# Kernel tuning notes

Measured on AMD Instinct MI355X. Metric: run time of the kernel, lower is better.

Reference implementation:

```python
import jax, jax.numpy as jnp
import numpy as np

B, C, H, W = 32, 256, 56, 56
NUM_ITER = 5

# Row-major upper-triangular (incl. diagonal) flat indices, matching
# torch.ones(C, C).triu().view(-1).nonzero() in the original triuvec.
_r, _c = np.triu_indices(C)
TRIU_IDX = jnp.asarray(_r * C + _c)


def setup_inputs() -> dict:
    key = jax.random.key(0)
    x = jax.random.normal(key, (B, C, H, W), dtype=jnp.float32)
    return {"x": x}


def _cov_pool(x):
    # x: (b, c, h, w) -> sigma = x_n @ ((1/n) I - (1/n^2) J) @ x_n^T : (b, c, c)
    b, c, h, w = x.shape
    n = h * w
    xn = x.reshape(b, c, n)
    s = xn.sum(axis=2)  # (b, c) = x_n @ ones
    gram = jnp.einsum('bcn,bdn->bcd', xn, xn)  # (b, c, c)
    return gram / n - jnp.einsum('bc,bd->bcd', s, s) / (n * n)


def _newton_schulz_sqrt(x, num_iter):
    # x: (b, m, m) SPD; returns approx matrix square root, scaled by sqrt(trace).
    b, m, _ = x.shape
    eye = jnp.eye(m, dtype=x.dtype)
    x_trace = jnp.trace(x, axis1=1, axis2=2)[:, None, None]  # (b, 1, 1)
    a = x / x_trace
    i3 = 3.0 * eye  # broadcasts over batch
    # iteration 0
    b2 = 0.5 * (i3 - a)
    yi = a @ b2
    zi = b2

    def body(carry, _):
        yi, zi = carry
        b2 = 0.5 * (i3 - zi @ yi)
        return (yi @ b2, b2 @ zi), None

    (yi, zi), _ = jax.lax.scan(body, (yi, zi), None, length=num_iter - 1)
    return yi * jnp.sqrt(x_trace)


def _triuvec(x):
    # (b, c, c) -> (b, c*(c+1)//2), row-major upper triangle incl. diagonal
    b, c, _ = x.shape
    return x.reshape(b, c * c)[:, TRIU_IDX]


def reference(x) -> jnp.ndarray:
    cov = _cov_pool(x)
    y = _newton_schulz_sqrt(cov, NUM_ITER)
    return _triuvec(y)
```

## Files before the change

### kernel.cpp

```cpp
#include <hip/hip_runtime.h>
#include <hip/hip_bf16.h>
#include <math.h>

#define BATCH 32
#define C 256
#define HW 3136
#define OUTROW 32896
#define KSPLIT 7
#define KCHUNK 448
#define KC32 98


typedef __bf16 b8v __attribute__((ext_vector_type(8)));
typedef float  f4v __attribute__((ext_vector_type(4)));

__device__ __forceinline__ unsigned short f2bf(float f) {
    union { float f; unsigned u; } v; v.f = f;
    unsigned r = v.u + 0x7FFFu + ((v.u >> 16) & 1u);
    return (unsigned short)(r >> 16);
}
__device__ __forceinline__ float bf2f(unsigned short h) {
    union { unsigned u; float f; } v; v.u = ((unsigned)h) << 16; return v.f;
}
__device__ __forceinline__ void split2(float x, unsigned short& h, unsigned short& l) {
    h = f2bf(x);
    l = f2bf(x - bf2f(h));
}

__device__ __forceinline__ float wave_sum(float v) {
    for (int o = 32; o; o >>= 1) v += __shfl_down(v, o, 64);
    return v;
}

__global__ void k_prep(const float* __restrict__ x, unsigned short* __restrict__ xh,
                       unsigned short* __restrict__ xl, float* __restrict__ sbuf,
                       float* __restrict__ qbuf) {
    const int row = blockIdx.x;
    const int b = row >> 8, c = row & 255;
    const float4* xr = (const float4*)(x + (size_t)row * HW);
    float s = 0.f, q = 0.f;
    for (int idx = threadIdx.x; idx < HW / 4; idx += 256) {
        const int k = idx * 4;
        const int kc = k >> 5, ko = k & 31;
        float4 v = xr[idx];
        ushort4 h, l;
        split2(v.x, h.x, l.x); split2(v.y, h.y, l.y);
        split2(v.z, h.z, l.z); split2(v.w, h.w, l.w);
        const size_t dst = ((size_t)(b * KC32 + kc) * 256 + c) * 32 + ko;
        *(ushort4*)&xh[dst] = h;
        *(ushort4*)&xl[dst] = l;
        s += v.x + v.y + v.z + v.w;
        q += v.x * v.x + v.y * v.y + v.z * v.z + v.w * v.w;
    }
    s = wave_sum(s); q = wave_sum(q);
    __shared__ float ss[4], qq[4];
    if ((threadIdx.x & 63) == 0) { ss[threadIdx.x >> 6] = s; qq[threadIdx.x >> 6] = q; }
    __syncthreads();
    if (threadIdx.x == 0) {
        sbuf[row] = ss[0] + ss[1] + ss[2] + ss[3];
        qbuf[row] = qq[0] + qq[1] + qq[2] + qq[3];
    }
}

__global__ void k_tr(const float* __restrict__ sbuf, const float* __restrict__ qbuf,
                     float* __restrict__ trbuf, float* __restrict__ strbuf) {
    const int b = blockIdx.x, t = threadIdx.x;
    const float invn = 1.f / (float)HW, invn2 = invn * invn;
    float sv = sbuf[b * C + t];
    float v = qbuf[b * C + t] * invn - sv * sv * invn2;
    v = wave_sum(v);
    __shared__ float red[4];
    if ((t & 63) == 0) red[t >> 6] = v;
    __syncthreads();
    if (t == 0) {
        float tr = red[0] + red[1] + red[2] + red[3];
        trbuf[b] = tr;
        strbuf[b] = sqrtf(tr);
    }
}

__global__ __launch_bounds__(64) void k_gram_split(
    const unsigned short* __restrict__ Xh, const unsigned short* __restrict__ Xl,
    float* __restrict__ part) {
    const int bid = blockIdx.x;
    const int x8 = bid & 7;
    const int t8 = bid >> 3;
    const int pairIdx = t8 % 10;
    const int g = (t8 / 10) * 8 + x8;
    const int b = g & 31;
    const int z = g >> 5;

    int p = pairIdx, tm = 0, rem = 4;
    while (p >= rem) { p -= rem; ++tm; --rem; }
    const int tn = tm + p;

    const int lane = threadIdx.x & 63;
    const int q = lane >> 4, r = lane & 15;
    const int kc0 = z * (KCHUNK / 32);
    const size_t matb = (size_t)b * KC32 * 8192;

    int oA[4], oB[4];
#pragma unroll
    for (int i = 0; i < 4; ++i) {
        oA[i] = (tm * 64 + i * 16 + r) * 32 + q * 8;
        oB[i] = (tn * 64 + i * 16 + r) * 32 + q * 8;
    }

    f4v acc[4][4] = {};
    b8v fAh[2][4], fAl[2][4], fBh[2][4], fBl[2][4];
#define LDG(buf, kc)                                                     \
    do {                                                                 \
        const size_t sb = matb + (size_t)(kc0 + (kc)) * 8192;            \
        for (int i = 0; i < 4; ++i) {                                    \
            fAh[buf][i] = *(const b8v*)(Xh + sb + oA[i]);                \
            fAl[buf][i] = *(const b8v*)(Xl + sb + oA[i]);                \
            fBh[buf][i] = *(const b8v*)(Xh + sb + oB[i]);                \
            fBl[buf][i] = *(const b8v*)(Xl + sb + oB[i]);                \
        }                                                                \
    } while (0)

    LDG(0, 0);
#pragma unroll
    for (int kc = 0; kc < KCHUNK / 32; ++kc) {
        const int cb = kc & 1, nb = cb ^ 1;
        if (kc < KCHUNK / 32 - 1) LDG(nb, kc + 1);
#pragma unroll
        for (int i = 0; i < 4; ++i)
#pragma unroll
            for (int j = 0; j < 4; ++j) {
                acc[i][j] = __builtin_amdgcn_mfma_f32_16x16x32_bf16(fAh[cb][i], fBh[cb][j], acc[i][j], 0, 0, 0);
                acc[i][j] = __builtin_amdgcn_mfma_f32_16x16x32_bf16(fAh[cb][i], fBl[cb][j], acc[i][j], 0, 0, 0);
                acc[i][j] = __builtin_amdgcn_mfma_f32_16x16x32_bf16(fAl[cb][i], fBh[cb][j], acc[i][j], 0, 0, 0);
            }
    }
#undef LDG

    float* pt = part + (((size_t)pairIdx * BATCH + b) * KSPLIT + z) * 4096;
#pragma unroll
    for (int i = 0; i < 4; ++i)
#pragma unroll
        for (int j = 0; j < 4; ++j)
#pragma unroll
            for (int reg = 0; reg < 4; ++reg) {
                int row = i * 16 + q * 4 + reg;
                int col = j * 16 + r;
                pt[row * 64 + col] = acc[i][j][reg];
            }
}

__global__ __launch_bounds__(256) void k_reduce(
    const float* __restrict__ part, const float* __restrict__ sbuf,
    const float* __restrict__ trbuf,
    unsigned short* __restrict__ Ahh, unsigned short* __restrict__ All,
    unsigned short* __restrict__ Zhh, unsigned short* __restrict__ Zll) {
    const int b = blockIdx.y;
    int p = blockIdx.x, tm = 0, rem = 4;
    while (p >= rem) { p -= rem; ++tm; --rem; }
    const int tn = tm + p;

    const float* pb = part + ((size_t)blockIdx.x * BATCH + b) * KSPLIT * 4096;
    const int t = threadIdx.x;
    const int row = t >> 2, c0 = (t & 3) * 16;

    float s[16];
#pragma unroll
    for (int u = 0; u < 16; ++u) s[u] = 0.f;
    for (int sp = 0; sp < KSPLIT; ++sp) {
        const float* q4 = pb + sp * 4096 + row * 64 + c0;
#pragma unroll
        for (int u4 = 0; u4 < 4; ++u4) {
            float4 v = *(const float4*)(q4 + u4 * 4);
            s[u4 * 4 + 0] += v.x; s[u4 * 4 + 1] += v.y;
            s[u4 * 4 + 2] += v.z; s[u4 * 4 + 3] += v.w;
        }
    }

    const float invn = 1.f / (float)HW, invn2 = invn * invn;
    const float tr = trbuf[b];
    const int gi = tm * 64 + row;
    const float si = sbuf[b * C + gi];
    const size_t mb = (size_t)b * 8 * 8192;

    __shared__ unsigned short tAh[64][66], tAl[64][66], tZh[64][66], tZl[64][66];
    unsigned short vAh[16], vAl[16], vZh[16], vZl[16];
#pragma unroll
    for (int u = 0; u < 16; ++u) {
        int gj = tn * 64 + c0 + u;
        float sj = sbuf[b * C + gj];
        float a = (s[u] * invn - si * sj * invn2) / tr;
        split2(a, vAh[u], vAl[u]);
        float zv = ((gi == gj) ? 1.5f : 0.f) - 0.5f * a;
        split2(zv, vZh[u], vZl[u]);
        tAh[row][c0 + u] = vAh[u]; tAl[row][c0 + u] = vAl[u];
        tZh[row][c0 + u] = vZh[u]; tZl[row][c0 + u] = vZl[u];
    }
#pragma unroll
    for (int u4 = 0; u4 < 4; ++u4) {
        const int col0 = tn * 64 + c0 + u4 * 4;
        const size_t off = mb + (size_t)(col0 >> 5) * 8192 + (size_t)gi * 32 + (col0 & 31);
        *(ushort4*)&Ahh[off] = *(ushort4*)&vAh[u4 * 4];
        *(ushort4*)&All[off] = *(ushort4*)&vAl[u4 * 4];
        *(ushort4*)&Zhh[off] = *(ushort4*)&vZh[u4 * 4];
        *(ushort4*)&Zll[off] = *(ushort4*)&vZl[u4 * 4];
    }
    if (tm != tn) {
        __syncthreads();
        const int mr = t >> 2, mc0 = (t & 3) * 16;
        const int gim = tn * 64 + mr;
        unsigned short wAh[16], wAl[16], wZh[16], wZl[16];
#pragma unroll
        for (int u = 0; u < 16; ++u) {
            wAh[u] = tAh[mc0 + u][mr]; wAl[u] = tAl[mc0 + u][mr];
            wZh[u] = tZh[mc0 + u][mr]; wZl[u] = tZl[mc0 + u][mr];
        }
#pragma unroll
        for (int u4 = 0; u4 < 4; ++u4) {
            const int col0 = tm * 64 + mc0 + u4 * 4;
            const size_t off = mb + (size_t)(col0 >> 5) * 8192 + (size_t)gim * 32 + (col0 & 31);
            *(ushort4*)&Ahh[off] = *(ushort4*)&wAh[u4 * 4];
            *(ushort4*)&All[off] = *(ushort4*)&wAl[u4 * 4];
            *(ushort4*)&Zhh[off] = *(ushort4*)&wZh[u4 * 4];
            *(ushort4*)&Zll[off] = *(ushort4*)&wZl[u4 * 4];
        }
    }
}

__device__ __forceinline__ void wave_gemm64(
    const unsigned short* __restrict__ Ah, const unsigned short* __restrict__ Al,
    const unsigned short* __restrict__ Bh, const unsigned short* __restrict__ Bl,
    int rowA, int rowB, f4v acc[4][4]) {
    const int lane = threadIdx.x & 63;
    const int q = lane >> 4, r = lane & 15;
    int oA[4], oB[4];
#pragma unroll
    for (int i = 0; i < 4; ++i) {
        oA[i] = (rowA + i * 16 + r) * 32 + q * 8;
        oB[i] = (rowB + i * 16 + r) * 32 + q * 8;
    }
    b8v fAh[2][4], fAl[2][4], fBh[2][4], fBl[2][4];
#define LD(buf, kc)                                              \
    do {                                                         \
        const size_t sb = (size_t)(kc) * 8192;                   \
        for (int i = 0; i < 4; ++i) {                            \
            fAh[buf][i] = *(const b8v*)(Ah + sb + oA[i]);        \
            fAl[buf][i] = *(const b8v*)(Al + sb + oA[i]);        \
            fBh[buf][i] = *(const b8v*)(Bh + sb + oB[i]);        \
            fBl[buf][i] = *(const b8v*)(Bl + sb + oB[i]);        \
        }                                                        \
    } while (0)

    LD(0, 0);
#pragma unroll
    for (int kc = 0; kc < 8; ++kc) {
        const int cb = kc & 1, nb = cb ^ 1;
        if (kc < 7) LD(nb, kc + 1);
#pragma unroll
        for (int i = 0; i < 4; ++i)
#pragma unroll
            for (int j = 0; j < 4; ++j) {
                acc[i][j] = __builtin_amdgcn_mfma_f32_16x16x32_bf16(fAh[cb][i], fBh[cb][j], acc[i][j], 0, 0, 0);
                acc[i][j] = __builtin_amdgcn_mfma_f32_16x16x32_bf16(fAh[cb][i], fBl[cb][j], acc[i][j], 0, 0, 0);
                acc[i][j] = __builtin_amdgcn_mfma_f32_16x16x32_bf16(fAl[cb][i], fBh[cb][j], acc[i][j], 0, 0, 0);
            }
    }
#undef LD
}

__device__ __forceinline__ void store_tile_fm(
    unsigned short* __restrict__ Dh, unsigned short* __restrict__ Dl,
    int tm, int tn, const f4v acc[4][4], bool modeT) {
    const int lane = threadIdx.x & 63, q = lane >> 4, r = lane & 15;
#pragma unroll
    for (int i = 0; i < 4; ++i)
#pragma unroll
        for (int j = 0; j < 4; ++j) {
            const int gj = tn * 64 + j * 16 + r;
            const size_t cbase = (size_t)(gj >> 5) * 8192 + (gj & 31);
#pragma unroll
            for (int reg = 0; reg < 4; ++reg) {
                const int gi = tm * 64 + i * 16 + q * 4 + reg;
                float v = acc[i][j][reg];
                if (modeT) v = ((gi == gj) ? 1.5f : 0.f) - 0.5f * v;
                unsigned short h, l;
                split2(v, h, l);
                Dh[cbase + (size_t)gi * 32] = h;
                Dl[cbase + (size_t)gi * 32] = l;
            }
        }
}

template <int MODE>
__global__ __launch_bounds__(64) void k_t64(
    const unsigned short* __restrict__ Ah, const unsigned short* __restrict__ Al,
    const unsigned short* __restrict__ Bh, const unsigned short* __restrict__ Bl,
    unsigned short* __restrict__ Dh, unsigned short* __restrict__ Dl,
    float* __restrict__ outF, const float* __restrict__ strbuf) {
    const int bid = blockIdx.x;
    const int x8 = bid & 7;
    const int w = bid >> 3;
    int b, tm, tn;
    if (MODE == 2) {
        b = x8 + 8 * (w / 10);
        int p = w % 10, rem = 4; tm = 0;
        while (p >= rem) { p -= rem; ++tm; --rem; }
        tn = tm + p;
    } else {
        b = x8 + 8 * (w >> 4);
        const int tile = w & 15;
        tm = tile >> 2; tn = tile & 3;
    }
    const size_t mo = (size_t)b * 8 * 8192;
    f4v acc[4][4] = {};
    wave_gemm64(Ah + mo, Al + mo, Bh + mo, Bl + mo, tm * 64, tn * 64, acc);

    if (MODE == 2) {
        const int lane = threadIdx.x & 63, q = lane >> 4, r = lane & 15;
        const float sc = strbuf[b];
#pragma unroll
        for (int i = 0; i < 4; ++i)
#pragma unroll
            for (int j = 0; j < 4; ++j) {
                const int gj = tn * 64 + j * 16 + r;
#pragma unroll
                for (int reg = 0; reg < 4; ++reg) {
                    const int gi = tm * 64 + i * 16 + q * 4 + reg;
                    if (gj >= gi)
                        outF[(size_t)b * OUTROW + (size_t)(gi * C - (gi * (gi - 1)) / 2) +
                             (gj - gi)] = acc[i][j][reg] * sc;
                }
            }
    } else {
        store_tile_fm(Dh + mo, Dl + mo, tm, tn, acc, MODE == 1);
    }
}

__global__ __launch_bounds__(64) void k_yz64(
    const unsigned short* __restrict__ Yh, const unsigned short* __restrict__ Yl,
    const unsigned short* __restrict__ Th, const unsigned short* __restrict__ Tl,
    const unsigned short* __restrict__ Zh, const unsigned short* __restrict__ Zl,
    unsigned short* __restrict__ Ynh, unsigned short* __restrict__ Ynl,
    unsigned short* __restrict__ Znh, unsigned short* __restrict__ Znl) {
    const int bid = blockIdx.x;
    const int x8 = bid & 7;
    const int w = bid >> 3;
    const int b = x8 + 8 * ((w >> 4) & 3);
    const int zz = w >> 6;
    const int tile = w & 15;
    const int tm = tile >> 2, tn = tile & 3;

    const unsigned short* Ah = zz ? Th : Yh;
    const unsigned short* Al = zz ? Tl : Yl;
    const unsigned short* Bh = zz ? Zh : Th;
    const unsigned short* Bl = zz ? Zl : Tl;
    unsigned short* Dh = zz ? Znh : Ynh;
    unsigned short* Dl = zz ? Znl : Ynl;

    const size_t mo = (size_t)b * 8 * 8192;
    f4v acc[4][4] = {};
    wave_gemm64(Ah + mo, Al + mo, Bh + mo, Bl + mo, tm * 64, tn * 64, acc);
    store_tile_fm(Dh + mo, Dl + mo, tm, tn, acc, false);
}

extern "C" void kernel_launch(void* const* d_in, const int* in_sizes, int n_in,
                              void* d_out, int out_size, void* d_ws, size_t ws_size,
                              hipStream_t stream) {
    const float* x = (const float*)d_in[0];
    float* out = (float*)d_out;

    unsigned short* W = (unsigned short*)d_ws;
    const size_t XN = (size_t)BATCH * C * HW;
    const size_t M = (size_t)BATCH * C * C;
    unsigned short* XH = W;
    unsigned short* XL = XH + XN;
    float* sbuf = (float*)(XL + XN);
    float* qbuf = sbuf + BATCH * C;
    float* trbuf = qbuf + BATCH * C;
    float* strbuf = trbuf + BATCH;
    unsigned short* P = (unsigned short*)(strbuf + BATCH);
    unsigned short* PA_h = P + 0 * M; unsigned short* PA_l = P + 1 * M;
    unsigned short* PB_h = P + 2 * M; unsigned short* PB_l = P + 3 * M;
    unsigned short* PC_h = P + 4 * M; unsigned short* PC_l = P + 5 * M;
    unsigned short* PD_h = P + 6 * M; unsigned short* PD_l = P + 7 * M;
    unsigned short* PE_h = P + 8 * M; unsigned short* PE_l = P + 9 * M;
    float* part = (float*)PC_h;

    k_prep<<<dim3(BATCH * C), 256, 0, stream>>>(x, XH, XL, sbuf, qbuf);
    k_tr<<<dim3(BATCH), 256, 0, stream>>>(sbuf, qbuf, trbuf, strbuf);
    k_gram_split<<<dim3(10 * BATCH * KSPLIT), 64, 0, stream>>>(XH, XL, part);
    k_reduce<<<dim3(10, BATCH), 256, 0, stream>>>(part, sbuf, trbuf,
                                                  PA_h, PA_l, PB_h, PB_l);

    dim3 g512(512);
    k_t64<0><<<g512, 64, 0, stream>>>(PA_h, PA_l, PB_h, PB_l, PC_h, PC_l, nullptr, strbuf);
    k_t64<1><<<g512, 64, 0, stream>>>(PB_h, PB_l, PC_h, PC_l, PD_h, PD_l, nullptr, strbuf);
    k_yz64<<<dim3(1024), 64, 0, stream>>>(PC_h, PC_l, PD_h, PD_l, PB_h, PB_l,
                                          PA_h, PA_l, PE_h, PE_l);
    k_t64<1><<<g512, 64, 0, stream>>>(PE_h, PE_l, PA_h, PA_l, PB_h, PB_l, nullptr, strbuf);
    k_yz64<<<dim3(1024), 64, 0, stream>>>(PA_h, PA_l, PB_h, PB_l, PE_h, PE_l,
                                          PC_h, PC_l, PD_h, PD_l);
    k_t64<1><<<g512, 64, 0, stream>>>(PD_h, PD_l, PC_h, PC_l, PA_h, PA_l, nullptr, strbuf);
    k_yz64<<<dim3(1024), 64, 0, stream>>>(PC_h, PC_l, PA_h, PA_l, PD_h, PD_l,
                                          PB_h, PB_l, PE_h, PE_l);
    k_t64<1><<<g512, 64, 0, stream>>>(PE_h, PE_l, PB_h, PB_l, PC_h, PC_l, nullptr, strbuf);
    k_t64<2><<<dim3(320), 64, 0, stream>>>(PB_h, PB_l, PC_h, PC_l, nullptr, nullptr,
                                           out, strbuf);
}
```

Before: 373.8 us.

## Restructure prep kernel to write contiguous k-chunk tiles with partial sums

The prep kernel now gives each block one (batch, 32-wide k-chunk) tile across all 256 channels instead of one channel row, so each thread writes a contiguous 8-element bf16 vector and the hi/lo output tile is written contiguously. Row sums and sums of squares become per-chunk partials in scratch buffers reused from the PA region, and the trace kernel reduces them over the 98 chunks. Reads of x become strided 32-byte segments per row, which trades read coalescing for write coalescing. It also adds a larger partial-sum reduction step in the trace kernel.

Measured after the change: 353.6 us. 1.06x faster.

```diff
diff --git a/kernel.cpp b/kernel.cpp
--- a/kernel.cpp
+++ b/kernel.cpp
@@ -13,6 +13,7 @@
 
 typedef __bf16 b8v __attribute__((ext_vector_type(8)));
 typedef float  f4v __attribute__((ext_vector_type(4)));
+typedef unsigned short u16x8 __attribute__((ext_vector_type(8)));
 
 __device__ __forceinline__ unsigned short f2bf(float f) {
     union { float f; unsigned u; } v; v.f = f;
@@ -32,42 +33,67 @@
     return v;
 }
 
-__global__ void k_prep(const float* __restrict__ x, unsigned short* __restrict__ xh,
-                       unsigned short* __restrict__ xl, float* __restrict__ sbuf,
-                       float* __restrict__ qbuf) {
-    const int row = blockIdx.x;
-    const int b = row >> 8, c = row & 255;
-    const float4* xr = (const float4*)(x + (size_t)row * HW);
+__global__ __launch_bounds__(256) void k_prep(const float* __restrict__ x,
+                                              unsigned short* __restrict__ xh,
+                                              unsigned short* __restrict__ xl,
+                                              float* __restrict__ psum,
+                                              float* __restrict__ qsum) {
+    const int blk = blockIdx.x;
+    const int b = blk / KC32;
+    const int kc = blk - b * KC32;
+    const int t = threadIdx.x;
+    const int lane4 = t & 3;
+    const int rowoff = t >> 2;
+    const int ko = lane4 * 8;
+
+    const float* xb = x + (size_t)b * C * HW + (size_t)kc * 32 + ko;
+    unsigned short* oh = xh + (size_t)blk * 8192 + ko;
+    unsigned short* ol = xl + (size_t)blk * 8192 + ko;
+    float* ps = psum + (size_t)blk * 256;
+    float* qs = qsum + (size_t)blk * 256;
+
+#pragma unroll
+    for (int it = 0; it < 4; ++it) {
+        const int row = it * 64 + rowoff;
+        const float* src = xb + (size_t)row * HW;
+        float4 v0 = *(const float4*)(src);
+        float4 v1 = *(const float4*)(src + 4);
+        float vv[8] = { v0.x, v0.y, v0.z, v0.w, v1.x, v1.y, v1.z, v1.w };
+        unsigned short ha[8], la[8];
+        float s = 0.f, q = 0.f;
+#pragma unroll
+        for (int j = 0; j < 8; ++j) {
+            split2(vv[j], ha[j], la[j]);
+            s += vv[j];
+            q = fmaf(vv[j], vv[j], q);
+        }
+        *(u16x8*)(oh + row * 32) = *(u16x8*)ha;
+        *(u16x8*)(ol + row * 32) = *(u16x8*)la;
+        s += __shfl_xor(s, 1, 64);
+        s += __shfl_xor(s, 2, 64);
+        q += __shfl_xor(q, 1, 64);
+        q += __shfl_xor(q, 2, 64);
+        if (lane4 == 0) { ps[row] = s; qs[row] = q; }
+    }
+}
+
+__global__ __launch_bounds__(256) void k_tr(const float* __restrict__ psum,
+                                            const float* __restrict__ qsum,
+                                            float* __restrict__ sbuf,
+                                            float* __restrict__ trbuf,
+                                            float* __restrict__ strbuf) {
+    const int b = blockIdx.x, t = threadIdx.x;
+    const float* ps = psum + (size_t)b * KC32 * 256 + t;
+    const float* qs = qsum + (size_t)b * KC32 * 256 + t;
     float s = 0.f, q = 0.f;
-    for (int idx = threadIdx.x; idx < HW / 4; idx += 256) {
-        const int k = idx * 4;
-        const int kc = k >> 5, ko = k & 31;
-        float4 v = xr[idx];
-        ushort4 h, l;
-        split2(v.x, h.x, l.x); split2(v.y, h.y, l.y);
-        split2(v.z, h.z, l.z); split2(v.w, h.w, l.w);
-        const size_t dst = ((size_t)(b * KC32 + kc) * 256 + c) * 32 + ko;
-        *(ushort4*)&xh[dst] = h;
-        *(ushort4*)&xl[dst] = l;
-        s += v.x + v.y + v.z + v.w;
-        q += v.x * v.x + v.y * v.y + v.z * v.z + v.w * v.w;
-    }
-    s = wave_sum(s); q = wave_sum(q);
-    __shared__ float ss[4], qq[4];
-    if ((threadIdx.x & 63) == 0) { ss[threadIdx.x >> 6] = s; qq[threadIdx.x >> 6] = q; }
-    __syncthreads();
-    if (threadIdx.x == 0) {
-        sbuf[row] = ss[0] + ss[1] + ss[2] + ss[3];
-        qbuf[row] = qq[0] + qq[1] + qq[2] + qq[3];
-    }
-}
-
-__global__ void k_tr(const float* __restrict__ sbuf, const float* __restrict__ qbuf,
-                     float* __restrict__ trbuf, float* __restrict__ strbuf) {
-    const int b = blockIdx.x, t = threadIdx.x;
+#pragma unroll 7
+    for (int kc = 0; kc < KC32; ++kc) {
+        s += ps[(size_t)kc * 256];
+        q += qs[(size_t)kc * 256];
+    }
+    sbuf[b * C + t] = s;
     const float invn = 1.f / (float)HW, invn2 = invn * invn;
-    float sv = sbuf[b * C + t];
-    float v = qbuf[b * C + t] * invn - sv * sv * invn2;
+    float v = q * invn - s * s * invn2;
     v = wave_sum(v);
     __shared__ float red[4];
     if ((t & 63) == 0) red[t >> 6] = v;
@@ -373,8 +399,7 @@
     unsigned short* XH = W;
     unsigned short* XL = XH + XN;
     float* sbuf = (float*)(XL + XN);
-    float* qbuf = sbuf + BATCH * C;
-    float* trbuf = qbuf + BATCH * C;
+    float* trbuf = sbuf + BATCH * C;
     float* strbuf = trbuf + BATCH;
     unsigned short* P = (unsigned short*)(strbuf + BATCH);
     unsigned short* PA_h = P + 0 * M; unsigned short* PA_l = P + 1 * M;
@@ -383,9 +408,11 @@
     unsigned short* PD_h = P + 6 * M; unsigned short* PD_l = P + 7 * M;
     unsigned short* PE_h = P + 8 * M; unsigned short* PE_l = P + 9 * M;
     float* part = (float*)PC_h;
-
-    k_prep<<<dim3(BATCH * C), 256, 0, stream>>>(x, XH, XL, sbuf, qbuf);
-    k_tr<<<dim3(BATCH), 256, 0, stream>>>(sbuf, qbuf, trbuf, strbuf);
+    float* psum = (float*)PA_h;
+    float* qsum = (float*)PA_l;
+
+    k_prep<<<dim3(BATCH * KC32), 256, 0, stream>>>(x, XH, XL, psum, qsum);
+    k_tr<<<dim3(BATCH), 256, 0, stream>>>(psum, qsum, sbuf, trbuf, strbuf);
     k_gram_split<<<dim3(10 * BATCH * KSPLIT), 64, 0, stream>>>(XH, XL, part);
     k_reduce<<<dim3(10, BATCH), 256, 0, stream>>>(part, sbuf, trbuf,
                                                   PA_h, PA_l, PB_h, PB_l);
```
